# Kernel optimization log

Measured on AMD Instinct MI355X. Metric: run time of the kernel, lower is better.

Reference implementation:

```python
import jax, jax.numpy as jnp
import numpy as np

N = 20000   # nodes/atoms
F = 256     # num_features
ORDER = 3   # order_in == order_out
# (l1, l2, L) triples: l1 < l2, |l1-l2| <= L <= min(l1+l2, order_out)
COMBOS = [(0,1,1),(0,2,2),(0,3,3),(1,2,1),(1,2,2),(1,2,3),(1,3,2),(1,3,3),(2,3,1),(2,3,2),(2,3,3)]


def setup_inputs() -> dict:
    key = jax.random.key(0)
    keys = iter(jax.random.split(key, 64))
    d = {}
    for l in range(ORDER + 1):
        d['x{}'.format(l)] = jax.random.normal(next(keys), (N, 2*l+1, F), dtype=jnp.float32)
    for L in range(ORDER + 1):
        d['keep{}'.format(L)] = jax.random.normal(next(keys), (F,), dtype=jnp.float32)
    for (l1, l2, L) in COMBOS:
        d['mix_{}_{}_{}'.format(l1, l2, L)] = jax.random.normal(next(keys), (F,), dtype=jnp.float32)
        d['cg_{}_{}_{}'.format(l1, l2, L)] = jax.random.normal(next(keys), (2*l1+1, 2*l2+1, 2*L+1), dtype=jnp.float32)
    return d


def reference(x0, x1, x2, x3,
              keep0, keep1, keep2, keep3,
              mix_0_1_1, mix_0_2_2, mix_0_3_3,
              mix_1_2_1, mix_1_2_2, mix_1_2_3,
              mix_1_3_2, mix_1_3_3,
              mix_2_3_1, mix_2_3_2, mix_2_3_3,
              cg_0_1_1, cg_0_2_2, cg_0_3_3,
              cg_1_2_1, cg_1_2_2, cg_1_2_3,
              cg_1_3_2, cg_1_3_3,
              cg_2_3_1, cg_2_3_2, cg_2_3_3):
    xs = [x0, x1, x2, x3]
    keeps = [keep0, keep1, keep2, keep3]
    mixes = {(0,1,1): mix_0_1_1, (0,2,2): mix_0_2_2, (0,3,3): mix_0_3_3,
             (1,2,1): mix_1_2_1, (1,2,2): mix_1_2_2, (1,2,3): mix_1_2_3,
             (1,3,2): mix_1_3_2, (1,3,3): mix_1_3_3,
             (2,3,1): mix_2_3_1, (2,3,2): mix_2_3_2, (2,3,3): mix_2_3_3}
    cgs = {(0,1,1): cg_0_1_1, (0,2,2): cg_0_2_2, (0,3,3): cg_0_3_3,
           (1,2,1): cg_1_2_1, (1,2,2): cg_1_2_2, (1,2,3): cg_1_2_3,
           (1,3,2): cg_1_3_2, (1,3,3): cg_1_3_3,
           (2,3,1): cg_2_3_1, (2,3,2): cg_2_3_2, (2,3,3): cg_2_3_3}
    # keep path: ys[L] = keepcoeff_L * xs[L]  (order_out == order_in, so no zero-pad branch)
    ys = [keeps[L] * xs[L] for L in range(ORDER + 1)]
    # mixing path: sum_{i,j} cg[i,j,k] * x_{l1}[n,i,f] * x_{l2}[n,j,f], scaled by per-feature mixcoeff
    for (l1, l2, L) in COMBOS:
        contrib = jnp.einsum('nif,njf,ijk->nkf', xs[l1], xs[l2], cgs[(l1, l2, L)])
        ys[L] = ys[L] + mixes[(l1, l2, L)] * contrib
    return tuple(ys)
```

## Files before the change

kernel.cpp:

```cpp
#include <hip/hip_runtime.h>
#include <stdint.h>

constexpr int NN = 20000;
constexpr int FF = 256;

typedef float v2f __attribute__((ext_vector_type(2)));

typedef const __attribute__((address_space(4))) float* cgp;
#define CGP(p) ((cgp)(uintptr_t)(p))

__device__ __forceinline__ v2f ld2(const float* p) {
    return *(const v2f*)p;
}
__device__ __forceinline__ void st2(float* p, v2f v) {
    *(v2f*)p = v;
}
__device__ __forceinline__ v2f pfma(v2f a, v2f b, v2f c) {
    return __builtin_elementwise_fma(a, b, c);
}
__device__ __forceinline__ v2f splat(float s) {
    v2f r = {s, s};
    return r;
}

__global__ __launch_bounds__(128, 2) void selfmix_kernel(
    const float* __restrict__ x0, const float* __restrict__ x1,
    const float* __restrict__ x2, const float* __restrict__ x3,
    const float* __restrict__ keep0, const float* __restrict__ keep1,
    const float* __restrict__ keep2, const float* __restrict__ keep3,
    const float* __restrict__ mix011, const float* __restrict__ cg011,
    const float* __restrict__ mix022, const float* __restrict__ cg022,
    const float* __restrict__ mix033, const float* __restrict__ cg033,
    const float* __restrict__ mix121, const float* __restrict__ cg121,
    const float* __restrict__ mix122, const float* __restrict__ cg122,
    const float* __restrict__ mix123, const float* __restrict__ cg123,
    const float* __restrict__ mix132, const float* __restrict__ cg132,
    const float* __restrict__ mix133, const float* __restrict__ cg133,
    const float* __restrict__ mix231, const float* __restrict__ cg231,
    const float* __restrict__ mix232, const float* __restrict__ cg232,
    const float* __restrict__ mix233, const float* __restrict__ cg233,
    float* __restrict__ out)
{
    const int n = blockIdx.x;
    const int fp = threadIdx.x;
    const int f2 = fp * 2;

    const v2f k0 = ld2(keep0 + f2), k1 = ld2(keep1 + f2);
    const v2f k2 = ld2(keep2 + f2), k3 = ld2(keep3 + f2);
    const v2f m011 = ld2(mix011 + f2), m022 = ld2(mix022 + f2), m033 = ld2(mix033 + f2);
    const v2f m121 = ld2(mix121 + f2), m122 = ld2(mix122 + f2), m123 = ld2(mix123 + f2);
    const v2f m132 = ld2(mix132 + f2), m133 = ld2(mix133 + f2);
    const v2f m231 = ld2(mix231 + f2), m232 = ld2(mix232 + f2), m233 = ld2(mix233 + f2);

    v2f a0 = ld2(x0 + n * FF + f2);
    v2f a1[3], a2[5], a3[7];
#pragma unroll
    for (int i = 0; i < 3; ++i) a1[i] = ld2(x1 + (n * 3 + i) * FF + f2);
#pragma unroll
    for (int i = 0; i < 5; ++i) a2[i] = ld2(x2 + (n * 5 + i) * FF + f2);
#pragma unroll
    for (int i = 0; i < 7; ++i) a3[i] = ld2(x3 + (n * 7 + i) * FF + f2);

    v2f y0 = k0 * a0;
    v2f y1[3], y2[5], y3[7];
#pragma unroll
    for (int i = 0; i < 3; ++i) y1[i] = k1 * a1[i];
#pragma unroll
    for (int i = 0; i < 5; ++i) y2[i] = k2 * a2[i];
#pragma unroll
    for (int i = 0; i < 7; ++i) y3[i] = k3 * a3[i];


    {
        cgp cg = CGP(cg011);
        v2f t[3] = {};
#pragma unroll
        for (int j = 0; j < 3; ++j) {
            const v2f p = a0 * a1[j];
#pragma unroll
            for (int k = 0; k < 3; ++k) t[k] = pfma(splat(cg[j * 3 + k]), p, t[k]);
        }
#pragma unroll
        for (int k = 0; k < 3; ++k) y1[k] = pfma(m011, t[k], y1[k]);
    }

    {
        cgp cg = CGP(cg022);
        v2f t[5] = {};
#pragma unroll
        for (int j = 0; j < 5; ++j) {
            const v2f p = a0 * a2[j];
#pragma unroll
            for (int k = 0; k < 5; ++k) t[k] = pfma(splat(cg[j * 5 + k]), p, t[k]);
        }
#pragma unroll
        for (int k = 0; k < 5; ++k) y2[k] = pfma(m022, t[k], y2[k]);
    }

    {
        cgp cg = CGP(cg033);
        v2f t[7] = {};
#pragma unroll
        for (int j = 0; j < 7; ++j) {
            const v2f p = a0 * a3[j];
#pragma unroll
            for (int k = 0; k < 7; ++k) t[k] = pfma(splat(cg[j * 7 + k]), p, t[k]);
        }
#pragma unroll
        for (int k = 0; k < 7; ++k) y3[k] = pfma(m033, t[k], y3[k]);
    }

    {
        cgp c1 = CGP(cg121);
        cgp c2 = CGP(cg122);
        cgp c3 = CGP(cg123);
        v2f t1[3] = {}, t2[5] = {}, t3[7] = {};
#pragma unroll
        for (int i = 0; i < 3; ++i) {
#pragma unroll
            for (int j = 0; j < 5; ++j) {
                const int ij = i * 5 + j;
                const v2f p = a1[i] * a2[j];
#pragma unroll
                for (int k = 0; k < 3; ++k) t1[k] = pfma(splat(c1[ij * 3 + k]), p, t1[k]);
#pragma unroll
                for (int k = 0; k < 5; ++k) t2[k] = pfma(splat(c2[ij * 5 + k]), p, t2[k]);
#pragma unroll
                for (int k = 0; k < 7; ++k) t3[k] = pfma(splat(c3[ij * 7 + k]), p, t3[k]);
            }
        }
#pragma unroll
        for (int k = 0; k < 3; ++k) y1[k] = pfma(m121, t1[k], y1[k]);
#pragma unroll
        for (int k = 0; k < 5; ++k) y2[k] = pfma(m122, t2[k], y2[k]);
#pragma unroll
        for (int k = 0; k < 7; ++k) y3[k] = pfma(m123, t3[k], y3[k]);
    }

    {
        cgp c2 = CGP(cg132);
        cgp c3 = CGP(cg133);
        v2f t2[5] = {}, t3[7] = {};
#pragma unroll
        for (int i = 0; i < 3; ++i) {
#pragma unroll
            for (int j = 0; j < 7; ++j) {
                const int ij = i * 7 + j;
                const v2f p = a1[i] * a3[j];
#pragma unroll
                for (int k = 0; k < 5; ++k) t2[k] = pfma(splat(c2[ij * 5 + k]), p, t2[k]);
#pragma unroll
                for (int k = 0; k < 7; ++k) t3[k] = pfma(splat(c3[ij * 7 + k]), p, t3[k]);
            }
        }
#pragma unroll
        for (int k = 0; k < 5; ++k) y2[k] = pfma(m132, t2[k], y2[k]);
#pragma unroll
        for (int k = 0; k < 7; ++k) y3[k] = pfma(m133, t3[k], y3[k]);
    }

    {
        cgp c1 = CGP(cg231);
        cgp c2 = CGP(cg232);
        cgp c3 = CGP(cg233);
        v2f t1[3] = {}, t2[5] = {}, t3[7] = {};
#pragma unroll
        for (int i = 0; i < 5; ++i) {
#pragma unroll
            for (int j = 0; j < 7; ++j) {
                const int ij = i * 7 + j;
                const v2f p = a2[i] * a3[j];
#pragma unroll
                for (int k = 0; k < 3; ++k) t1[k] = pfma(splat(c1[ij * 3 + k]), p, t1[k]);
#pragma unroll
                for (int k = 0; k < 5; ++k) t2[k] = pfma(splat(c2[ij * 5 + k]), p, t2[k]);
#pragma unroll
                for (int k = 0; k < 7; ++k) t3[k] = pfma(splat(c3[ij * 7 + k]), p, t3[k]);
            }
        }
#pragma unroll
        for (int k = 0; k < 3; ++k) y1[k] = pfma(m231, t1[k], y1[k]);
#pragma unroll
        for (int k = 0; k < 5; ++k) y2[k] = pfma(m232, t2[k], y2[k]);
#pragma unroll
        for (int k = 0; k < 7; ++k) y3[k] = pfma(m233, t3[k], y3[k]);
    }

    float* o0 = out;
    float* o1 = out + (size_t)NN * FF;
    float* o2 = out + (size_t)NN * 4 * FF;
    float* o3 = out + (size_t)NN * 9 * FF;

    st2(o0 + n * FF + f2, y0);
#pragma unroll
    for (int k = 0; k < 3; ++k) st2(o1 + (n * 3 + k) * FF + f2, y1[k]);
#pragma unroll
    for (int k = 0; k < 5; ++k) st2(o2 + (n * 5 + k) * FF + f2, y2[k]);
#pragma unroll
    for (int k = 0; k < 7; ++k) st2(o3 + (n * 7 + k) * FF + f2, y3[k]);
}

extern "C" void kernel_launch(void* const* d_in, const int* in_sizes, int n_in,
                              void* d_out, int out_size, void* d_ws, size_t ws_size,
                              hipStream_t stream) {
    const float* x0 = (const float*)d_in[0];
    const float* x1 = (const float*)d_in[1];
    const float* x2 = (const float*)d_in[2];
    const float* x3 = (const float*)d_in[3];
    const float* keep0 = (const float*)d_in[4];
    const float* keep1 = (const float*)d_in[5];
    const float* keep2 = (const float*)d_in[6];
    const float* keep3 = (const float*)d_in[7];
    const float* mix011 = (const float*)d_in[8];
    const float* cg011  = (const float*)d_in[9];
    const float* mix022 = (const float*)d_in[10];
    const float* cg022  = (const float*)d_in[11];
    const float* mix033 = (const float*)d_in[12];
    const float* cg033  = (const float*)d_in[13];
    const float* mix121 = (const float*)d_in[14];
    const float* cg121  = (const float*)d_in[15];
    const float* mix122 = (const float*)d_in[16];
    const float* cg122  = (const float*)d_in[17];
    const float* mix123 = (const float*)d_in[18];
    const float* cg123  = (const float*)d_in[19];
    const float* mix132 = (const float*)d_in[20];
    const float* cg132  = (const float*)d_in[21];
    const float* mix133 = (const float*)d_in[22];
    const float* cg133  = (const float*)d_in[23];
    const float* mix231 = (const float*)d_in[24];
    const float* cg231  = (const float*)d_in[25];
    const float* mix232 = (const float*)d_in[26];
    const float* cg232  = (const float*)d_in[27];
    const float* mix233 = (const float*)d_in[28];
    const float* cg233  = (const float*)d_in[29];

    dim3 grid(NN);
    dim3 block(FF / 2);
    hipLaunchKernelGGL(selfmix_kernel, grid, block, 0, stream,
                       x0, x1, x2, x3,
                       keep0, keep1, keep2, keep3,
                       mix011, cg011, mix022, cg022, mix033, cg033,
                       mix121, cg121, mix122, cg122, mix123, cg123,
                       mix132, cg132, mix133, cg133,
                       mix231, cg231, mix232, cg232, mix233, cg233,
                       (float*)d_out);
}
```

Baseline: 161.7 us.

## Map one node per wave with four features per lane and scalar-operand FMAs

Each wavefront now handles a whole node, with each lane covering four features using 128-bit loads and stores. Blocks hold four nodes, so the grid shrinks fourfold. The packed v2 FMAs with splatted coefficients become inline-asm scalar v_fma_f32 that take the CG coefficient from an SGPR, and the first term of each accumulator is a multiply instead of an FMA into zero. Wider per-lane vectors raise register pressure, and occupancy is pinned to two waves per EU, which may limit latency hiding; the inline asm also blocks the compiler from forming packed FMAs.

```diff
diff --git a/kernel.cpp b/kernel.cpp
--- a/kernel.cpp
+++ b/kernel.cpp
@@ -3,27 +3,49 @@
 
 constexpr int NN = 20000;
 constexpr int FF = 256;
-
-typedef float v2f __attribute__((ext_vector_type(2)));
+constexpr int NODES_PER_BLOCK = 4;
+
+typedef float v4f __attribute__((ext_vector_type(4)));
 
 typedef const __attribute__((address_space(4))) float* cgp;
 #define CGP(p) ((cgp)(uintptr_t)(p))
 
-__device__ __forceinline__ v2f ld2(const float* p) {
-    return *(const v2f*)p;
-}
-__device__ __forceinline__ void st2(float* p, v2f v) {
-    *(v2f*)p = v;
-}
-__device__ __forceinline__ v2f pfma(v2f a, v2f b, v2f c) {
+__device__ __forceinline__ v4f ld4(const float* p) { return *(const v4f*)p; }
+__device__ __forceinline__ void st4(float* p, v4f v) { *(v4f*)p = v; }
+
+__device__ __forceinline__ float sfma(float c, float p, float acc) {
+    float d;
+    asm("v_fma_f32 %0, %1, %2, %3" : "=v"(d) : "s"(c), "v"(p), "v"(acc));
+    return d;
+}
+__device__ __forceinline__ float smul(float c, float p) {
+    float d;
+    asm("v_mul_f32 %0, %1, %2" : "=v"(d) : "s"(c), "v"(p));
+    return d;
+}
+
+template<int DO>
+__device__ __forceinline__ void addk(cgp cg, int ijDO, v4f p, v4f* t, bool first) {
+#pragma unroll
+    for (int k = 0; k < DO; ++k) {
+        const float c = cg[ijDO + k];
+        if (first) {
+            t[k].x = smul(c, p.x); t[k].y = smul(c, p.y);
+            t[k].z = smul(c, p.z); t[k].w = smul(c, p.w);
+        } else {
+            t[k].x = sfma(c, p.x, t[k].x); t[k].y = sfma(c, p.y, t[k].y);
+            t[k].z = sfma(c, p.z, t[k].z); t[k].w = sfma(c, p.w, t[k].w);
+        }
+    }
+}
+
+__device__ __forceinline__ v4f vfma(v4f a, v4f b, v4f c) {
     return __builtin_elementwise_fma(a, b, c);
 }
-__device__ __forceinline__ v2f splat(float s) {
-    v2f r = {s, s};
-    return r;
-}
-
-__global__ __launch_bounds__(128, 2) void selfmix_kernel(
+
+__global__ void __launch_bounds__(256)
+__attribute__((amdgpu_waves_per_eu(2, 2)))
+selfmix_kernel(
     const float* __restrict__ x0, const float* __restrict__ x1,
     const float* __restrict__ x2, const float* __restrict__ x3,
     const float* __restrict__ keep0, const float* __restrict__ keep1,
@@ -41,149 +63,136 @@
     const float* __restrict__ mix233, const float* __restrict__ cg233,
     float* __restrict__ out)
 {
-    const int n = blockIdx.x;
-    const int fp = threadIdx.x;
-    const int f2 = fp * 2;
-
-    const v2f k0 = ld2(keep0 + f2), k1 = ld2(keep1 + f2);
-    const v2f k2 = ld2(keep2 + f2), k3 = ld2(keep3 + f2);
-    const v2f m011 = ld2(mix011 + f2), m022 = ld2(mix022 + f2), m033 = ld2(mix033 + f2);
-    const v2f m121 = ld2(mix121 + f2), m122 = ld2(mix122 + f2), m123 = ld2(mix123 + f2);
-    const v2f m132 = ld2(mix132 + f2), m133 = ld2(mix133 + f2);
-    const v2f m231 = ld2(mix231 + f2), m232 = ld2(mix232 + f2), m233 = ld2(mix233 + f2);
-
-    v2f a0 = ld2(x0 + n * FF + f2);
-    v2f a1[3], a2[5], a3[7];
-#pragma unroll
-    for (int i = 0; i < 3; ++i) a1[i] = ld2(x1 + (n * 3 + i) * FF + f2);
-#pragma unroll
-    for (int i = 0; i < 5; ++i) a2[i] = ld2(x2 + (n * 5 + i) * FF + f2);
-#pragma unroll
-    for (int i = 0; i < 7; ++i) a3[i] = ld2(x3 + (n * 7 + i) * FF + f2);
-
-    v2f y0 = k0 * a0;
-    v2f y1[3], y2[5], y3[7];
-#pragma unroll
-    for (int i = 0; i < 3; ++i) y1[i] = k1 * a1[i];
-#pragma unroll
-    for (int i = 0; i < 5; ++i) y2[i] = k2 * a2[i];
-#pragma unroll
-    for (int i = 0; i < 7; ++i) y3[i] = k3 * a3[i];
-
-
-    {
+    const int wid  = threadIdx.x >> 6;
+    const int lane = threadIdx.x & 63;
+    const int n    = blockIdx.x * NODES_PER_BLOCK + wid;
+    const int f0   = lane * 4;
+
+    v4f a0 = ld4(x0 + n * FF + f0);
+    v4f a1[3], a2[5], a3[7];
+#pragma unroll
+    for (int i = 0; i < 3; ++i) a1[i] = ld4(x1 + (n * 3 + i) * FF + f0);
+#pragma unroll
+    for (int i = 0; i < 5; ++i) a2[i] = ld4(x2 + (n * 5 + i) * FF + f0);
+#pragma unroll
+    for (int i = 0; i < 7; ++i) a3[i] = ld4(x3 + (n * 7 + i) * FF + f0);
+
+    v4f y0 = ld4(keep0 + f0) * a0;
+    v4f y1[3], y2[5], y3[7];
+    {
+        const v4f k1 = ld4(keep1 + f0);
+#pragma unroll
+        for (int i = 0; i < 3; ++i) y1[i] = k1 * a1[i];
+        const v4f k2 = ld4(keep2 + f0);
+#pragma unroll
+        for (int i = 0; i < 5; ++i) y2[i] = k2 * a2[i];
+        const v4f k3 = ld4(keep3 + f0);
+#pragma unroll
+        for (int i = 0; i < 7; ++i) y3[i] = k3 * a3[i];
+    }
+
+    {
+        const v4f m = ld4(mix011 + f0);
         cgp cg = CGP(cg011);
-        v2f t[3] = {};
-#pragma unroll
-        for (int j = 0; j < 3; ++j) {
-            const v2f p = a0 * a1[j];
-#pragma unroll
-            for (int k = 0; k < 3; ++k) t[k] = pfma(splat(cg[j * 3 + k]), p, t[k]);
-        }
-#pragma unroll
-        for (int k = 0; k < 3; ++k) y1[k] = pfma(m011, t[k], y1[k]);
-    }
-
-    {
+        v4f t[3];
+#pragma unroll
+        for (int j = 0; j < 3; ++j)
+            addk<3>(cg, j * 3, a0 * a1[j], t, j == 0);
+#pragma unroll
+        for (int k = 0; k < 3; ++k) y1[k] = vfma(m, t[k], y1[k]);
+    }
+
+    {
+        const v4f m = ld4(mix022 + f0);
         cgp cg = CGP(cg022);
-        v2f t[5] = {};
-#pragma unroll
-        for (int j = 0; j < 5; ++j) {
-            const v2f p = a0 * a2[j];
-#pragma unroll
-            for (int k = 0; k < 5; ++k) t[k] = pfma(splat(cg[j * 5 + k]), p, t[k]);
-        }
-#pragma unroll
-        for (int k = 0; k < 5; ++k) y2[k] = pfma(m022, t[k], y2[k]);
-    }
-
-    {
+        v4f t[5];
+#pragma unroll
+        for (int j = 0; j < 5; ++j)
+            addk<5>(cg, j * 5, a0 * a2[j], t, j == 0);
+#pragma unroll
+        for (int k = 0; k < 5; ++k) y2[k] = vfma(m, t[k], y2[k]);
+    }
+
+    {
+        const v4f m = ld4(mix033 + f0);
         cgp cg = CGP(cg033);
-        v2f t[7] = {};
-#pragma unroll
-        for (int j = 0; j < 7; ++j) {
-            const v2f p = a0 * a3[j];
-#pragma unroll
-            for (int k = 0; k < 7; ++k) t[k] = pfma(splat(cg[j * 7 + k]), p, t[k]);
-        }
-#pragma unroll
-        for (int k = 0; k < 7; ++k) y3[k] = pfma(m033, t[k], y3[k]);
-    }
-
-    {
+        v4f t[7];
+#pragma unroll
+        for (int j = 0; j < 7; ++j)
+            addk<7>(cg, j * 7, a0 * a3[j], t, j == 0);
+#pragma unroll
+        for (int k = 0; k < 7; ++k) y3[k] = vfma(m, t[k], y3[k]);
+    }
+
+    {
+        const v4f mA = ld4(mix121 + f0), mB = ld4(mix122 + f0), mC = ld4(mix123 + f0);
         cgp c1 = CGP(cg121);
         cgp c2 = CGP(cg122);
         cgp c3 = CGP(cg123);
-        v2f t1[3] = {}, t2[5] = {}, t3[7] = {};
+        v4f t1[3], t2[5], t3[7];
 #pragma unroll
         for (int i = 0; i < 3; ++i) {
 #pragma unroll
             for (int j = 0; j < 5; ++j) {
                 const int ij = i * 5 + j;
-                const v2f p = a1[i] * a2[j];
-#pragma unroll
-                for (int k = 0; k < 3; ++k) t1[k] = pfma(splat(c1[ij * 3 + k]), p, t1[k]);
-#pragma unroll
-                for (int k = 0; k < 5; ++k) t2[k] = pfma(splat(c2[ij * 5 + k]), p, t2[k]);
-#pragma unroll
-                for (int k = 0; k < 7; ++k) t3[k] = pfma(splat(c3[ij * 7 + k]), p, t3[k]);
+                const v4f p = a1[i] * a2[j];
+                addk<3>(c1, ij * 3, p, t1, ij == 0);
+                addk<5>(c2, ij * 5, p, t2, ij == 0);
+                addk<7>(c3, ij * 7, p, t3, ij == 0);
             }
         }
 #pragma unroll
-        for (int k = 0; k < 3; ++k) y1[k] = pfma(m121, t1[k], y1[k]);
-#pragma unroll
-        for (int k = 0; k < 5; ++k) y2[k] = pfma(m122, t2[k], y2[k]);
-#pragma unroll
-        for (int k = 0; k < 7; ++k) y3[k] = pfma(m123, t3[k], y3[k]);
-    }
-
-    {
+        for (int k = 0; k < 3; ++k) y1[k] = vfma(mA, t1[k], y1[k]);
+#pragma unroll
+        for (int k = 0; k < 5; ++k) y2[k] = vfma(mB, t2[k], y2[k]);
+#pragma unroll
+        for (int k = 0; k < 7; ++k) y3[k] = vfma(mC, t3[k], y3[k]);
+    }
+
+    {
+        const v4f mB = ld4(mix132 + f0), mC = ld4(mix133 + f0);
         cgp c2 = CGP(cg132);
         cgp c3 = CGP(cg133);
-        v2f t2[5] = {}, t3[7] = {};
+        v4f t2[5], t3[7];
 #pragma unroll
         for (int i = 0; i < 3; ++i) {
 #pragma unroll
             for (int j = 0; j < 7; ++j) {
                 const int ij = i * 7 + j;
-                const v2f p = a1[i] * a3[j];
-#pragma unroll
-                for (int k = 0; k < 5; ++k) t2[k] = pfma(splat(c2[ij * 5 + k]), p, t2[k]);
-#pragma unroll
-                for (int k = 0; k < 7; ++k) t3[k] = pfma(splat(c3[ij * 7 + k]), p, t3[k]);
+                const v4f p = a1[i] * a3[j];
+                addk<5>(c2, ij * 5, p, t2, ij == 0);
+                addk<7>(c3, ij * 7, p, t3, ij == 0);
             }
         }
 #pragma unroll
-        for (int k = 0; k < 5; ++k) y2[k] = pfma(m132, t2[k], y2[k]);
-#pragma unroll
-        for (int k = 0; k < 7; ++k) y3[k] = pfma(m133, t3[k], y3[k]);
-    }
-
-    {
+        for (int k = 0; k < 5; ++k) y2[k] = vfma(mB, t2[k], y2[k]);
+#pragma unroll
+        for (int k = 0; k < 7; ++k) y3[k] = vfma(mC, t3[k], y3[k]);
+    }
+
+    {
+        const v4f mA = ld4(mix231 + f0), mB = ld4(mix232 + f0), mC = ld4(mix233 + f0);
         cgp c1 = CGP(cg231);
         cgp c2 = CGP(cg232);
         cgp c3 = CGP(cg233);
-        v2f t1[3] = {}, t2[5] = {}, t3[7] = {};
+        v4f t1[3], t2[5], t3[7];
 #pragma unroll
         for (int i = 0; i < 5; ++i) {
 #pragma unroll
             for (int j = 0; j < 7; ++j) {
                 const int ij = i * 7 + j;
-                const v2f p = a2[i] * a3[j];
-#pragma unroll
-                for (int k = 0; k < 3; ++k) t1[k] = pfma(splat(c1[ij * 3 + k]), p, t1[k]);
-#pragma unroll
-                for (int k = 0; k < 5; ++k) t2[k] = pfma(splat(c2[ij * 5 + k]), p, t2[k]);
-#pragma unroll
-                for (int k = 0; k < 7; ++k) t3[k] = pfma(splat(c3[ij * 7 + k]), p, t3[k]);
+                const v4f p = a2[i] * a3[j];
+                addk<3>(c1, ij * 3, p, t1, ij == 0);
+                addk<5>(c2, ij * 5, p, t2, ij == 0);
+                addk<7>(c3, ij * 7, p, t3, ij == 0);
             }
         }
 #pragma unroll
-        for (int k = 0; k < 3; ++k) y1[k] = pfma(m231, t1[k], y1[k]);
-#pragma unroll
-        for (int k = 0; k < 5; ++k) y2[k] = pfma(m232, t2[k], y2[k]);
-#pragma unroll
-        for (int k = 0; k < 7; ++k) y3[k] = pfma(m233, t3[k], y3[k]);
+        for (int k = 0; k < 3; ++k) y1[k] = vfma(mA, t1[k], y1[k]);
+#pragma unroll
+        for (int k = 0; k < 5; ++k) y2[k] = vfma(mB, t2[k], y2[k]);
+#pragma unroll
+        for (int k = 0; k < 7; ++k) y3[k] = vfma(mC, t3[k], y3[k]);
     }
 
     float* o0 = out;
@@ -191,13 +200,13 @@
     float* o2 = out + (size_t)NN * 4 * FF;
     float* o3 = out + (size_t)NN * 9 * FF;
 
-    st2(o0 + n * FF + f2, y0);
-#pragma unroll
-    for (int k = 0; k < 3; ++k) st2(o1 + (n * 3 + k) * FF + f2, y1[k]);
-#pragma unroll
-    for (int k = 0; k < 5; ++k) st2(o2 + (n * 5 + k) * FF + f2, y2[k]);
-#pragma unroll
-    for (int k = 0; k < 7; ++k) st2(o3 + (n * 7 + k) * FF + f2, y3[k]);
+    st4(o0 + n * FF + f0, y0);
+#pragma unroll
+    for (int k = 0; k < 3; ++k) st4(o1 + (n * 3 + k) * FF + f0, y1[k]);
+#pragma unroll
+    for (int k = 0; k < 5; ++k) st4(o2 + (n * 5 + k) * FF + f0, y2[k]);
+#pragma unroll
+    for (int k = 0; k < 7; ++k) st4(o3 + (n * 7 + k) * FF + f0, y3[k]);
 }
 
 extern "C" void kernel_launch(void* const* d_in, const int* in_sizes, int n_in,
@@ -234,8 +243,8 @@
     const float* mix233 = (const float*)d_in[28];
     const float* cg233  = (const float*)d_in[29];
 
-    dim3 grid(NN);
-    dim3 block(FF / 2);
+    dim3 grid(NN / NODES_PER_BLOCK);
+    dim3 block(256);
     hipLaunchKernelGGL(selfmix_kernel, grid, block, 0, stream,
                        x0, x1, x2, x3,
                        keep0, keep1, keep2, keep3,
```

After: 315.1 us. 1.95x slower.
